# Kernel optimization log

Measured on AMD Instinct MI355X. Metric: run time of the kernel, lower is better.

Reference implementation:

```python
import jax, jax.numpy as jnp
import numpy as np

NB_HEAD = 16
SIZE_PER_HEAD = 64
D_MODEL = 1024
B, SQ, SK = 4, 2048, 2048


def setup_inputs() -> dict:
    key = jax.random.key(0)
    ks = jax.random.split(key, 8)
    Q_seq = jax.random.normal(ks[0], (B, SQ, D_MODEL), dtype=jnp.float32)
    K_seq = jax.random.normal(ks[1], (B, SK, D_MODEL), dtype=jnp.float32)
    V_seq = jax.random.normal(ks[2], (B, SK, D_MODEL), dtype=jnp.float32)
    Q_len = jax.random.randint(ks[3], (B, 1), 0, SQ, dtype=jnp.int32)
    V_len = jax.random.randint(ks[4], (B, 1), 0, SK, dtype=jnp.int32)
    out_dim = NB_HEAD * SIZE_PER_HEAD
    scale = float(np.sqrt(6.0 / (D_MODEL + out_dim)))  # glorot_uniform
    WQ = jax.random.uniform(ks[5], (D_MODEL, out_dim), jnp.float32, -scale, scale)
    WK = jax.random.uniform(ks[6], (D_MODEL, out_dim), jnp.float32, -scale, scale)
    WV = jax.random.uniform(ks[7], (D_MODEL, out_dim), jnp.float32, -scale, scale)
    return {"Q_seq": Q_seq, "K_seq": K_seq, "V_seq": V_seq,
            "Q_len": Q_len, "V_len": V_len, "WQ": WQ, "WK": WK, "WV": WV}


def reference(Q_seq, K_seq, V_seq, Q_len, V_len, WQ, WK, WV):
    b, sq, _ = Q_seq.shape
    sk = K_seq.shape[1]
    H, D = NB_HEAD, SIZE_PER_HEAD
    # projections -> [B, H, S, D]
    Q = (Q_seq @ WQ).reshape(b, sq, H, D).transpose(0, 2, 1, 3)
    K = (K_seq @ WK).reshape(b, sk, H, D).transpose(0, 2, 1, 3)
    V = (V_seq @ WV).reshape(b, sk, H, D).transpose(0, 2, 1, 3)
    # scaled dot-product scores [B, H, Sq, Sk]
    A = jnp.einsum('bhqd,bhkd->bhqk', Q, K) / jnp.float32(np.sqrt(D))
    # faithful to original Mask (no cumsum): masks ONLY the key position == V_len
    vmask = jax.nn.one_hot(V_len[:, 0], sk, dtype=A.dtype)  # [B, Sk]
    A = A - vmask[:, None, None, :] * jnp.float32(1e12)
    A = jax.nn.softmax(A, axis=-1)
    out = jnp.einsum('bhqk,bhkd->bhqd', A, V)
    out = out.transpose(0, 2, 1, 3).reshape(b, sq, H * D)
    # multiplicative mask: zeros ONLY the query position == Q_len
    qmask = 1.0 - jax.nn.one_hot(Q_len[:, 0], sq, dtype=out.dtype)  # [B, Sq]
    return out * qmask[:, :, None]
```

## Files before the change

kernel.cpp:

```cpp
#include <hip/hip_runtime.h>
#include <hip/hip_bf16.h>

typedef float f32x4 __attribute__((ext_vector_type(4)));
typedef float f32x16 __attribute__((ext_vector_type(16)));
typedef short bf16x8 __attribute__((ext_vector_type(8)));
typedef unsigned short u16;
typedef u16 u16x4 __attribute__((ext_vector_type(4)));
typedef u16 u16x8 __attribute__((ext_vector_type(8)));
typedef unsigned u32;
typedef unsigned u32x2 __attribute__((ext_vector_type(2)));

#define GLDS(gp, lp) __builtin_amdgcn_global_load_lds( \
    (const __attribute__((address_space(1))) void*)(gp), \
    (__attribute__((address_space(3))) void*)(lp), 16, 0, 0)

__device__ __forceinline__ u16 f2bf(float f) {
  union { float f; unsigned u; } v; v.f = f;
  unsigned r = v.u + 0x7fffu + ((v.u >> 16) & 1u);
  return (u16)(r >> 16);
}

__device__ __forceinline__ u32 cvtpk(float lo, float hi) {
  u32 r;
  asm("v_cvt_pk_bf16_f32 %0, %1, %2" : "=v"(r) : "v"(lo), "v"(hi));
  return r;
}

__device__ __forceinline__ float exp2i(float x) {
  float r;
  asm("v_exp_f32 %0, %1" : "=v"(r) : "v"(x));
  return r;
}

__global__ __launch_bounds__(256) void ktrans(const float* __restrict__ WQ,
                                              const float* __restrict__ WK,
                                              const float* __restrict__ WV,
                                              u16* __restrict__ Wt) {
  int z = blockIdx.z;
  const float* W = (z == 0) ? WQ : (z == 1) ? WK : WV;
  u16* o = Wt + (size_t)z * 1024 * 1024;
  float scale = (z == 0) ? 0.18033688f : 1.0f;
  __shared__ float tl[32][33];
  int tx = threadIdx.x & 31, ty = threadIdx.x >> 5;
  int ko = blockIdx.x * 32, no = blockIdx.y * 32;
#pragma unroll
  for (int i = 0; i < 32; i += 8)
    tl[ty + i][tx] = W[(size_t)(ko + ty + i) * 1024 + no + tx];
  __syncthreads();
#pragma unroll
  for (int i = 0; i < 32; i += 8)
    o[(size_t)(no + ty + i) * 1024 + ko + tx] = f2bf(tl[tx][ty + i] * scale);
}

__global__ __launch_bounds__(256) void kconv(const float* __restrict__ A, u16* __restrict__ Ab) {
  int tid = blockIdx.x * 256 + threadIdx.x;
  size_t base = (size_t)tid * 16;
  const f32x4* p = (const f32x4*)(A + base);
  f32x4 v0 = p[0], v1 = p[1], v2 = p[2], v3 = p[3];
  union { u32 u[8]; u16x8 h[2]; } pk;
  pk.u[0] = cvtpk(v0.x, v0.y); pk.u[1] = cvtpk(v0.z, v0.w);
  pk.u[2] = cvtpk(v1.x, v1.y); pk.u[3] = cvtpk(v1.z, v1.w);
  pk.u[4] = cvtpk(v2.x, v2.y); pk.u[5] = cvtpk(v2.z, v2.w);
  pk.u[6] = cvtpk(v3.x, v3.y); pk.u[7] = cvtpk(v3.z, v3.w);
  *(u16x8*)(Ab + base) = pk.h[0];
  *(u16x8*)(Ab + base + 8) = pk.h[1];
}

__global__ __launch_bounds__(256, 3) void kproj(
    const u16* __restrict__ Ab, const u16* __restrict__ Wz,
    u16* __restrict__ O, int isV) {
  __shared__ __align__(16) u16 lds[16384];
  int t = threadIdx.x, lane = t & 63, w = t >> 6;
  int wm = (w >> 1) * 64, wn = (w & 1) * 64;
  int f = blockIdx.y * 8 + blockIdx.x;
  int x_t = (f >> 3) & 7;
  int y_t = (f & 7) | ((f >> 6) << 3);
  int m0 = y_t * 128, n0 = x_t * 128;
  f32x4 acc[4][4];
#pragma unroll
  for (int i = 0; i < 4; ++i)
#pragma unroll
    for (int j = 0; j < 4; ++j) acc[i][j] = (f32x4){0.f, 0.f, 0.f, 0.f};

  int srow = t >> 3, sk8 = (t & 7) << 3;
  int lbw = w * 512;
  const u16* gA = Ab + (size_t)(m0 + srow) * 1024 + (sk8 ^ ((srow & 7) << 3));
  const u16* gB = Wz + (size_t)(n0 + srow) * 1024 + (sk8 ^ ((srow & 7) << 3));

  for (int k0 = 0; k0 < 1024; k0 += 64) {
    __syncthreads();
#pragma unroll
    for (int p = 0; p < 4; ++p) GLDS(gA + p * 32768 + k0, &lds[p * 2048 + lbw]);
#pragma unroll
    for (int p = 0; p < 4; ++p) GLDS(gB + p * 32768 + k0, &lds[8192 + p * 2048 + lbw]);
    __syncthreads();
#pragma unroll
    for (int kk = 0; kk < 64; kk += 32) {
      int ko8 = kk + ((lane >> 4) << 3);
      bf16x8 af[4], bfr[4];
#pragma unroll
      for (int mi = 0; mi < 4; ++mi) {
        int r = wm + mi * 16 + (lane & 15);
        af[mi] = *(const bf16x8*)(&lds[r * 64 + (ko8 ^ ((r & 7) << 3))]);
      }
#pragma unroll
      for (int ni = 0; ni < 4; ++ni) {
        int r = wn + ni * 16 + (lane & 15);
        bfr[ni] = *(const bf16x8*)(&lds[8192 + r * 64 + (ko8 ^ ((r & 7) << 3))]);
      }
#pragma unroll
      for (int mi = 0; mi < 4; ++mi)
#pragma unroll
        for (int ni = 0; ni < 4; ++ni)
          acc[mi][ni] = __builtin_amdgcn_mfma_f32_16x16x32_bf16(af[mi], bfr[ni], acc[mi][ni], 0, 0, 0);
    }
  }
  int bb = m0 >> 11;
  if (!isV) {
#pragma unroll
    for (int mi = 0; mi < 4; ++mi) {
      int m4 = m0 + wm + mi * 16 + ((lane >> 4) << 2);
      int s4 = m4 & 2047;
#pragma unroll
      for (int ni = 0; ni < 4; ++ni) {
        int n = n0 + wn + ni * 16 + (lane & 15);
        int hh = n >> 6, d = n & 63;
        u16* op = O + (((size_t)(bb * 16 + hh) * 2048 + s4) * 64 + d);
#pragma unroll
        for (int j = 0; j < 4; ++j) op[(size_t)j * 64] = f2bf(acc[mi][ni][j]);
      }
    }
  } else {
#pragma unroll
    for (int mi = 0; mi < 4; ++mi) {
      int m4 = m0 + wm + mi * 16 + ((lane >> 4) << 2);
      int s4 = m4 & 2047;
#pragma unroll
      for (int ni = 0; ni < 4; ++ni) {
        int n = n0 + wn + ni * 16 + (lane & 15);
        int hh = n >> 6, d = n & 63;
        u16x4 pv = {f2bf(acc[mi][ni][0]), f2bf(acc[mi][ni][1]),
                    f2bf(acc[mi][ni][2]), f2bf(acc[mi][ni][3])};
        *(u16x4*)(&O[((size_t)(bb * 16 + hh) * 64 + d) * 2048 + s4]) = pv;
      }
    }
  }
}

__global__ __launch_bounds__(512, 4) void kattn(
    const u16* __restrict__ Qw, const u16* __restrict__ Kw, const u16* __restrict__ Vt,
    const int* __restrict__ Qlen, const int* __restrict__ Vlen, float* __restrict__ out) {
  int fid = blockIdx.x;
  int bh = (fid & 7) * 8 + (fid >> 6);
  int qx = (fid >> 3) & 7;
  int b = bh >> 4, h = bh & 15;
  int q0 = qx * 256;
  int t = threadIdx.x, lane = t & 63, w = t >> 6, hi = lane >> 5, ln = lane & 31;
  __shared__ __align__(16) u16 smem[16384];
  const int qlen = Qlen[b], vlen = Vlen[b];

  const u16* Qp = Qw + ((size_t)bh * 2048 + q0 + w * 32 + ln) * 64;
  bf16x8 qf[4];
#pragma unroll
  for (int r = 0; r < 4; ++r) qf[r] = *(const bf16x8*)(Qp + r * 16 + hi * 8);

  int srow = t >> 3;
  int sks = (((t & 7) << 4) ^ ((srow & 7) << 4)) >> 1;
  const u16* gK = Kw + ((size_t)bh * 2048 + srow) * 64 + sks;
  const u16* gV = Vt + ((size_t)bh * 64 + srow) * 2048 + sks;
  int lbw = (t >> 6) * 512;

  GLDS(gK, &smem[lbw]);
  GLDS(gV, &smem[4096 + lbw]);

  float Lloc = 0.f;
  f32x16 o0, o1;
#pragma unroll
  for (int i = 0; i < 16; ++i) { o0[i] = 0.f; o1[i] = 0.f; }
  __syncthreads();

  for (int kt = 0; kt < 32; ++kt) {
    int qb = (kt & 1) * 8192;
    int nb = ((kt & 1) ^ 1) * 8192;
    if (kt < 31) {
      GLDS(gK + (size_t)(kt + 1) * 4096, &smem[nb + lbw]);
      GLDS(gV + (kt + 1) * 64, &smem[nb + 4096 + lbw]);
    }
    f32x16 sa[2];
#pragma unroll
    for (int kb = 0; kb < 2; ++kb)
#pragma unroll
      for (int i = 0; i < 16; ++i) sa[kb][i] = 0.f;
    __builtin_amdgcn_s_setprio(1);
#pragma unroll
    for (int kb = 0; kb < 2; ++kb) {
      int row = kb * 32 + ln;
      int rs7 = (row & 7) << 4;
#pragma unroll
      for (int r = 0; r < 4; ++r) {
        int byt = row * 128 + ((r * 32 + hi * 16) ^ rs7);
        bf16x8 kf = *(const bf16x8*)(&smem[qb + (byt >> 1)]);
        sa[kb] = __builtin_amdgcn_mfma_f32_32x32x16_bf16(kf, qf[r], sa[kb], 0, 0, 0);
      }
    }
    __builtin_amdgcn_s_setprio(0);
    if ((vlen >> 6) == kt) {
#pragma unroll
      for (int kb = 0; kb < 2; ++kb)
#pragma unroll
        for (int i = 0; i < 16; ++i) {
          int kv = (kt << 6) + kb * 32 + ((i & 3) + ((i >> 2) << 3)) + (hi << 2);
          if (kv == vlen) sa[kb][i] = -1e12f;
        }
    }
    float r0 = 0.f, r1 = 0.f, r2 = 0.f, r3 = 0.f;
#pragma unroll
    for (int kb = 0; kb < 2; ++kb)
#pragma unroll
      for (int i = 0; i < 16; i += 4) {
        float p0 = exp2i(sa[kb][i]);     sa[kb][i] = p0;     r0 += p0;
        float p1 = exp2i(sa[kb][i + 1]); sa[kb][i + 1] = p1; r1 += p1;
        float p2 = exp2i(sa[kb][i + 2]); sa[kb][i + 2] = p2; r2 += p2;
        float p3 = exp2i(sa[kb][i + 3]); sa[kb][i + 3] = p3; r3 += p3;
      }
    Lloc += (r0 + r1) + (r2 + r3);
    bf16x8 pf[4];
#pragma unroll
    for (int kb = 0; kb < 2; ++kb)
#pragma unroll
      for (int ff = 0; ff < 2; ++ff) {
        u32 a0 = cvtpk(sa[kb][8 * ff + 0], sa[kb][8 * ff + 1]);
        u32 b0 = cvtpk(sa[kb][8 * ff + 4], sa[kb][8 * ff + 5]);
        u32x2 q0v = __builtin_amdgcn_permlane32_swap(a0, b0, false, false);
        u32 a1 = cvtpk(sa[kb][8 * ff + 2], sa[kb][8 * ff + 3]);
        u32 b1 = cvtpk(sa[kb][8 * ff + 6], sa[kb][8 * ff + 7]);
        u32x2 q1v = __builtin_amdgcn_permlane32_swap(a1, b1, false, false);
        union { u32 u[4]; bf16x8 v; } uu;
        uu.u[0] = q0v.x; uu.u[1] = q1v.x; uu.u[2] = q0v.y; uu.u[3] = q1v.y;
        pf[kb * 2 + ff] = uu.v;
      }
    __builtin_amdgcn_s_setprio(1);
#pragma unroll
    for (int db = 0; db < 2; ++db) {
      int row = db * 32 + ln;
      int rs7 = (row & 7) << 4;
#pragma unroll
      for (int s4 = 0; s4 < 4; ++s4) {
        int byt = row * 128 + ((s4 * 32 + hi * 16) ^ rs7);
        bf16x8 vf = *(const bf16x8*)(&smem[qb + 4096 + (byt >> 1)]);
        if (db == 0) o0 = __builtin_amdgcn_mfma_f32_32x32x16_bf16(vf, pf[s4], o0, 0, 0, 0);
        else         o1 = __builtin_amdgcn_mfma_f32_32x32x16_bf16(vf, pf[s4], o1, 0, 0, 0);
      }
    }
    __builtin_amdgcn_s_setprio(0);
    __syncthreads();
  }
  float Lt = Lloc + __shfl_xor(Lloc, 32, 64);
  int q = q0 + w * 32 + ln;
  float inv = (q == qlen) ? 0.f : 1.f / Lt;
  float* op = out + ((size_t)b * 2048 + q) * 1024 + h * 64;
#pragma unroll
  for (int g = 0; g < 4; ++g) {
    f32x4 v0 = {o0[4 * g + 0] * inv, o0[4 * g + 1] * inv, o0[4 * g + 2] * inv, o0[4 * g + 3] * inv};
    *(f32x4*)(op + g * 8 + hi * 4) = v0;
    f32x4 v1 = {o1[4 * g + 0] * inv, o1[4 * g + 1] * inv, o1[4 * g + 2] * inv, o1[4 * g + 3] * inv};
    *(f32x4*)(op + 32 + g * 8 + hi * 4) = v1;
  }
}

extern "C" void kernel_launch(void* const* d_in, const int* in_sizes, int n_in,
                              void* d_out, int out_size, void* d_ws, size_t ws_size,
                              hipStream_t stream) {
  (void)in_sizes; (void)n_in; (void)out_size; (void)ws_size;
  const float* Qs = (const float*)d_in[0];
  const float* Ks = (const float*)d_in[1];
  const float* Vs = (const float*)d_in[2];
  const int* Ql = (const int*)d_in[3];
  const int* Vl = (const int*)d_in[4];
  const float* WQ = (const float*)d_in[5];
  const float* WK = (const float*)d_in[6];
  const float* WV = (const float*)d_in[7];
  float* out = (float*)d_out;

  const size_t M1 = 1024 * 1024;
  u16* Wt = (u16*)d_ws;
  u16* Qw = Wt + 3 * M1;
  u16* Kw = Qw + 8 * M1;
  u16* Vtw = Kw + 8 * M1;
  u16* Ab = Vtw + 8 * M1;

  ktrans<<<dim3(32, 32, 3), 256, 0, stream>>>(WQ, WK, WV, Wt);
  kconv<<<2048, 256, 0, stream>>>(Qs, Ab);
  kproj<<<dim3(8, 64), 256, 0, stream>>>(Ab, Wt, Qw, 0);
  kconv<<<2048, 256, 0, stream>>>(Ks, Ab);
  kproj<<<dim3(8, 64), 256, 0, stream>>>(Ab, Wt + M1, Kw, 0);
  kconv<<<2048, 256, 0, stream>>>(Vs, Ab);
  kproj<<<dim3(8, 64), 256, 0, stream>>>(Ab, Wt + 2 * M1, Vtw, 1);
  kattn<<<512, 512, 0, stream>>>(Qw, Kw, Vtw, Ql, Vl, out);
}
```

Measured before the change: 303.3 us.

## Batch Q/K/V conversion and projection launches; deepen attention K/V prefetch to two tiles

The three conversion kernels and three projection GEMMs are merged into single launches indexed by a grid dimension. The bf16 copies of Q and K inputs are staged in the output buffer so all three can live at once. In the attention kernel, each pipeline stage now loads two 64-key K/V tiles, doubling LDS to 64KB and halving the number of block barriers. Fewer launches and fuller grids should cut launch gaps and tail effects, but the larger LDS footprint may reduce attention occupancy.

```diff
diff --git a/kernel.cpp b/kernel.cpp
--- a/kernel.cpp
+++ b/kernel.cpp
@@ -52,7 +52,15 @@
     o[(size_t)(no + ty + i) * 1024 + ko + tx] = f2bf(tl[tx][ty + i] * scale);
 }
 
-__global__ __launch_bounds__(256) void kconv(const float* __restrict__ A, u16* __restrict__ Ab) {
+__global__ __launch_bounds__(256) void kconv3(const float* __restrict__ A0,
+                                              const float* __restrict__ A1,
+                                              const float* __restrict__ A2,
+                                              u16* __restrict__ B0,
+                                              u16* __restrict__ B1,
+                                              u16* __restrict__ B2) {
+  int z = blockIdx.y;
+  const float* A = (z == 0) ? A0 : (z == 1) ? A1 : A2;
+  u16* Ab = (z == 0) ? B0 : (z == 1) ? B1 : B2;
   int tid = blockIdx.x * 256 + threadIdx.x;
   size_t base = (size_t)tid * 16;
   const f32x4* p = (const f32x4*)(A + base);
@@ -67,8 +75,13 @@
 }
 
 __global__ __launch_bounds__(256, 3) void kproj(
-    const u16* __restrict__ Ab, const u16* __restrict__ Wz,
-    u16* __restrict__ O, int isV) {
+    const u16* __restrict__ Ab0, const u16* __restrict__ Ab1, const u16* __restrict__ Ab2,
+    const u16* __restrict__ Wt, u16* __restrict__ Qw, u16* __restrict__ Kw,
+    u16* __restrict__ Vtw) {
+  int z = blockIdx.z;
+  const u16* Ab = (z == 0) ? Ab0 : (z == 1) ? Ab1 : Ab2;
+  const u16* Wz = Wt + (size_t)z * 1024 * 1024;
+  u16* O = (z == 0) ? Qw : (z == 1) ? Kw : Vtw;
   __shared__ __align__(16) u16 lds[16384];
   int t = threadIdx.x, lane = t & 63, w = t >> 6;
   int wm = (w >> 1) * 64, wn = (w & 1) * 64;
@@ -116,7 +129,7 @@
     }
   }
   int bb = m0 >> 11;
-  if (!isV) {
+  if (z < 2) {
 #pragma unroll
     for (int mi = 0; mi < 4; ++mi) {
       int m4 = m0 + wm + mi * 16 + ((lane >> 4) << 2);
@@ -156,7 +169,7 @@
   int b = bh >> 4, h = bh & 15;
   int q0 = qx * 256;
   int t = threadIdx.x, lane = t & 63, w = t >> 6, hi = lane >> 5, ln = lane & 31;
-  __shared__ __align__(16) u16 smem[16384];
+  __shared__ __align__(16) u16 smem[32768];
   const int qlen = Qlen[b], vlen = Vlen[b];
 
   const u16* Qp = Qw + ((size_t)bh * 2048 + q0 + w * 32 + ln) * 64;
@@ -172,6 +185,8 @@
 
   GLDS(gK, &smem[lbw]);
   GLDS(gV, &smem[4096 + lbw]);
+  GLDS(gK + 4096, &smem[8192 + lbw]);
+  GLDS(gV + 64, &smem[12288 + lbw]);
 
   float Lloc = 0.f;
   f32x16 o0, o1;
@@ -179,80 +194,87 @@
   for (int i = 0; i < 16; ++i) { o0[i] = 0.f; o1[i] = 0.f; }
   __syncthreads();
 
-  for (int kt = 0; kt < 32; ++kt) {
-    int qb = (kt & 1) * 8192;
-    int nb = ((kt & 1) ^ 1) * 8192;
-    if (kt < 31) {
-      GLDS(gK + (size_t)(kt + 1) * 4096, &smem[nb + lbw]);
-      GLDS(gV + (kt + 1) * 64, &smem[nb + 4096 + lbw]);
-    }
-    f32x16 sa[2];
-#pragma unroll
-    for (int kb = 0; kb < 2; ++kb)
-#pragma unroll
-      for (int i = 0; i < 16; ++i) sa[kb][i] = 0.f;
-    __builtin_amdgcn_s_setprio(1);
-#pragma unroll
-    for (int kb = 0; kb < 2; ++kb) {
-      int row = kb * 32 + ln;
-      int rs7 = (row & 7) << 4;
-#pragma unroll
-      for (int r = 0; r < 4; ++r) {
-        int byt = row * 128 + ((r * 32 + hi * 16) ^ rs7);
-        bf16x8 kf = *(const bf16x8*)(&smem[qb + (byt >> 1)]);
-        sa[kb] = __builtin_amdgcn_mfma_f32_32x32x16_bf16(kf, qf[r], sa[kb], 0, 0, 0);
-      }
-    }
-    __builtin_amdgcn_s_setprio(0);
-    if ((vlen >> 6) == kt) {
+  for (int kt = 0; kt < 16; ++kt) {
+    int qb = (kt & 1) << 14;
+    int nb = qb ^ 16384;
+    if (kt < 15) {
+      GLDS(gK + (size_t)(2 * kt + 2) * 4096, &smem[nb + lbw]);
+      GLDS(gV + (2 * kt + 2) * 64, &smem[nb + 4096 + lbw]);
+      GLDS(gK + (size_t)(2 * kt + 3) * 4096, &smem[nb + 8192 + lbw]);
+      GLDS(gV + (2 * kt + 3) * 64, &smem[nb + 12288 + lbw]);
+    }
+#pragma unroll
+    for (int u = 0; u < 2; ++u) {
+      int tb = qb + u * 8192;
+      int tau = 2 * kt + u;
+      f32x16 sa[2];
 #pragma unroll
       for (int kb = 0; kb < 2; ++kb)
 #pragma unroll
-        for (int i = 0; i < 16; ++i) {
-          int kv = (kt << 6) + kb * 32 + ((i & 3) + ((i >> 2) << 3)) + (hi << 2);
-          if (kv == vlen) sa[kb][i] = -1e12f;
+        for (int i = 0; i < 16; ++i) sa[kb][i] = 0.f;
+      __builtin_amdgcn_s_setprio(1);
+#pragma unroll
+      for (int kb = 0; kb < 2; ++kb) {
+        int row = kb * 32 + ln;
+        int rs7 = (row & 7) << 4;
+#pragma unroll
+        for (int r = 0; r < 4; ++r) {
+          int byt = row * 128 + ((r * 32 + hi * 16) ^ rs7);
+          bf16x8 kf = *(const bf16x8*)(&smem[tb + (byt >> 1)]);
+          sa[kb] = __builtin_amdgcn_mfma_f32_32x32x16_bf16(kf, qf[r], sa[kb], 0, 0, 0);
         }
-    }
-    float r0 = 0.f, r1 = 0.f, r2 = 0.f, r3 = 0.f;
-#pragma unroll
-    for (int kb = 0; kb < 2; ++kb)
-#pragma unroll
-      for (int i = 0; i < 16; i += 4) {
-        float p0 = exp2i(sa[kb][i]);     sa[kb][i] = p0;     r0 += p0;
-        float p1 = exp2i(sa[kb][i + 1]); sa[kb][i + 1] = p1; r1 += p1;
-        float p2 = exp2i(sa[kb][i + 2]); sa[kb][i + 2] = p2; r2 += p2;
-        float p3 = exp2i(sa[kb][i + 3]); sa[kb][i + 3] = p3; r3 += p3;
-      }
-    Lloc += (r0 + r1) + (r2 + r3);
-    bf16x8 pf[4];
-#pragma unroll
-    for (int kb = 0; kb < 2; ++kb)
-#pragma unroll
-      for (int ff = 0; ff < 2; ++ff) {
-        u32 a0 = cvtpk(sa[kb][8 * ff + 0], sa[kb][8 * ff + 1]);
-        u32 b0 = cvtpk(sa[kb][8 * ff + 4], sa[kb][8 * ff + 5]);
-        u32x2 q0v = __builtin_amdgcn_permlane32_swap(a0, b0, false, false);
-        u32 a1 = cvtpk(sa[kb][8 * ff + 2], sa[kb][8 * ff + 3]);
-        u32 b1 = cvtpk(sa[kb][8 * ff + 6], sa[kb][8 * ff + 7]);
-        u32x2 q1v = __builtin_amdgcn_permlane32_swap(a1, b1, false, false);
-        union { u32 u[4]; bf16x8 v; } uu;
-        uu.u[0] = q0v.x; uu.u[1] = q1v.x; uu.u[2] = q0v.y; uu.u[3] = q1v.y;
-        pf[kb * 2 + ff] = uu.v;
-      }
-    __builtin_amdgcn_s_setprio(1);
-#pragma unroll
-    for (int db = 0; db < 2; ++db) {
-      int row = db * 32 + ln;
-      int rs7 = (row & 7) << 4;
-#pragma unroll
-      for (int s4 = 0; s4 < 4; ++s4) {
-        int byt = row * 128 + ((s4 * 32 + hi * 16) ^ rs7);
-        bf16x8 vf = *(const bf16x8*)(&smem[qb + 4096 + (byt >> 1)]);
-        if (db == 0) o0 = __builtin_amdgcn_mfma_f32_32x32x16_bf16(vf, pf[s4], o0, 0, 0, 0);
-        else         o1 = __builtin_amdgcn_mfma_f32_32x32x16_bf16(vf, pf[s4], o1, 0, 0, 0);
-      }
-    }
-    __builtin_amdgcn_s_setprio(0);
+      }
+      __builtin_amdgcn_s_setprio(0);
+      if ((vlen >> 6) == tau) {
+#pragma unroll
+        for (int kb = 0; kb < 2; ++kb)
+#pragma unroll
+          for (int i = 0; i < 16; ++i) {
+            int kv = (tau << 6) + kb * 32 + ((i & 3) + ((i >> 2) << 3)) + (hi << 2);
+            if (kv == vlen) sa[kb][i] = -1e12f;
+          }
+      }
+      float r0 = 0.f, r1 = 0.f, r2 = 0.f, r3 = 0.f;
+#pragma unroll
+      for (int kb = 0; kb < 2; ++kb)
+#pragma unroll
+        for (int i = 0; i < 16; i += 4) {
+          float p0 = exp2i(sa[kb][i]);     sa[kb][i] = p0;     r0 += p0;
+          float p1 = exp2i(sa[kb][i + 1]); sa[kb][i + 1] = p1; r1 += p1;
+          float p2 = exp2i(sa[kb][i + 2]); sa[kb][i + 2] = p2; r2 += p2;
+          float p3 = exp2i(sa[kb][i + 3]); sa[kb][i + 3] = p3; r3 += p3;
+        }
+      Lloc += (r0 + r1) + (r2 + r3);
+      bf16x8 pf[4];
+#pragma unroll
+      for (int kb = 0; kb < 2; ++kb)
+#pragma unroll
+        for (int ff = 0; ff < 2; ++ff) {
+          u32 a0 = cvtpk(sa[kb][8 * ff + 0], sa[kb][8 * ff + 1]);
+          u32 b0 = cvtpk(sa[kb][8 * ff + 4], sa[kb][8 * ff + 5]);
+          u32x2 q0v = __builtin_amdgcn_permlane32_swap(a0, b0, false, false);
+          u32 a1 = cvtpk(sa[kb][8 * ff + 2], sa[kb][8 * ff + 3]);
+          u32 b1 = cvtpk(sa[kb][8 * ff + 6], sa[kb][8 * ff + 7]);
+          u32x2 q1v = __builtin_amdgcn_permlane32_swap(a1, b1, false, false);
+          union { u32 u[4]; bf16x8 v; } uu;
+          uu.u[0] = q0v.x; uu.u[1] = q1v.x; uu.u[2] = q0v.y; uu.u[3] = q1v.y;
+          pf[kb * 2 + ff] = uu.v;
+        }
+      __builtin_amdgcn_s_setprio(1);
+#pragma unroll
+      for (int db = 0; db < 2; ++db) {
+        int row = db * 32 + ln;
+        int rs7 = (row & 7) << 4;
+#pragma unroll
+        for (int s4 = 0; s4 < 4; ++s4) {
+          int byt = row * 128 + ((s4 * 32 + hi * 16) ^ rs7);
+          bf16x8 vf = *(const bf16x8*)(&smem[tb + 4096 + (byt >> 1)]);
+          if (db == 0) o0 = __builtin_amdgcn_mfma_f32_32x32x16_bf16(vf, pf[s4], o0, 0, 0, 0);
+          else         o1 = __builtin_amdgcn_mfma_f32_32x32x16_bf16(vf, pf[s4], o1, 0, 0, 0);
+        }
+      }
+      __builtin_amdgcn_s_setprio(0);
+    }
     __syncthreads();
   }
   float Lt = Lloc + __shfl_xor(Lloc, 32, 64);
@@ -287,14 +309,12 @@
   u16* Qw = Wt + 3 * M1;
   u16* Kw = Qw + 8 * M1;
   u16* Vtw = Kw + 8 * M1;
-  u16* Ab = Vtw + 8 * M1;
+  u16* Ab2 = Vtw + 8 * M1;
+  u16* Ab0 = (u16*)d_out;
+  u16* Ab1 = Ab0 + 8 * M1;
 
   ktrans<<<dim3(32, 32, 3), 256, 0, stream>>>(WQ, WK, WV, Wt);
-  kconv<<<2048, 256, 0, stream>>>(Qs, Ab);
-  kproj<<<dim3(8, 64), 256, 0, stream>>>(Ab, Wt, Qw, 0);
-  kconv<<<2048, 256, 0, stream>>>(Ks, Ab);
-  kproj<<<dim3(8, 64), 256, 0, stream>>>(Ab, Wt + M1, Kw, 0);
-  kconv<<<2048, 256, 0, stream>>>(Vs, Ab);
-  kproj<<<dim3(8, 64), 256, 0, stream>>>(Ab, Wt + 2 * M1, Vtw, 1);
+  kconv3<<<dim3(2048, 3), 256, 0, stream>>>(Qs, Ks, Vs, Ab0, Ab1, Ab2);
+  kproj<<<dim3(8, 64, 3), 256, 0, stream>>>(Ab0, Ab1, Ab2, Wt, Qw, Kw, Vtw);
   kattn<<<512, 512, 0, stream>>>(Qw, Kw, Vtw, Ql, Vl, out);
 }
```

New measurement: 312.9 us. 1.03x slower.

## Fuse fp32-to-bf16 activation conversion into projection GEMM and batch three projections

Applied to the files above, without the earlier changes.

Removes the separate conversion kernels that wrote bf16 copies of Q/K/V inputs, instead loading fp32 tiles into LDS via global_load_lds and converting to bf16 when building MFMA fragments. The three projection GEMMs are launched as one grid using blockIdx.z. This avoids writing and re-reading intermediate bf16 buffers and two launches, at the cost of larger LDS usage, doubled A-tile global bytes, and redundant per-block conversions.

```diff
diff --git a/kernel.cpp b/kernel.cpp
--- a/kernel.cpp
+++ b/kernel.cpp
@@ -52,24 +52,16 @@
     o[(size_t)(no + ty + i) * 1024 + ko + tx] = f2bf(tl[tx][ty + i] * scale);
 }
 
-__global__ __launch_bounds__(256) void kconv(const float* __restrict__ A, u16* __restrict__ Ab) {
-  int tid = blockIdx.x * 256 + threadIdx.x;
-  size_t base = (size_t)tid * 16;
-  const f32x4* p = (const f32x4*)(A + base);
-  f32x4 v0 = p[0], v1 = p[1], v2 = p[2], v3 = p[3];
-  union { u32 u[8]; u16x8 h[2]; } pk;
-  pk.u[0] = cvtpk(v0.x, v0.y); pk.u[1] = cvtpk(v0.z, v0.w);
-  pk.u[2] = cvtpk(v1.x, v1.y); pk.u[3] = cvtpk(v1.z, v1.w);
-  pk.u[4] = cvtpk(v2.x, v2.y); pk.u[5] = cvtpk(v2.z, v2.w);
-  pk.u[6] = cvtpk(v3.x, v3.y); pk.u[7] = cvtpk(v3.z, v3.w);
-  *(u16x8*)(Ab + base) = pk.h[0];
-  *(u16x8*)(Ab + base + 8) = pk.h[1];
-}
-
 __global__ __launch_bounds__(256, 3) void kproj(
-    const u16* __restrict__ Ab, const u16* __restrict__ Wz,
-    u16* __restrict__ O, int isV) {
-  __shared__ __align__(16) u16 lds[16384];
+    const float* __restrict__ A0, const float* __restrict__ A1, const float* __restrict__ A2,
+    const u16* __restrict__ Wt, u16* __restrict__ Qw, u16* __restrict__ Kw,
+    u16* __restrict__ Vtw) {
+  int z = blockIdx.z;
+  const float* A = (z == 0) ? A0 : (z == 1) ? A1 : A2;
+  const u16* Wz = Wt + (size_t)z * 1024 * 1024;
+  u16* O = (z == 0) ? Qw : (z == 1) ? Kw : Vtw;
+  __shared__ __align__(16) float ldsA[8192];
+  __shared__ __align__(16) u16 ldsB[8192];
   int t = threadIdx.x, lane = t & 63, w = t >> 6;
   int wm = (w >> 1) * 64, wn = (w & 1) * 64;
   int f = blockIdx.y * 8 + blockIdx.x;
@@ -82,17 +74,19 @@
 #pragma unroll
     for (int j = 0; j < 4; ++j) acc[i][j] = (f32x4){0.f, 0.f, 0.f, 0.f};
 
+  int srow16 = t >> 4, sk4 = (t & 15) << 2;
   int srow = t >> 3, sk8 = (t & 7) << 3;
-  int lbw = w * 512;
-  const u16* gA = Ab + (size_t)(m0 + srow) * 1024 + (sk8 ^ ((srow & 7) << 3));
+  const float* gA = A + (size_t)(m0 + srow16) * 1024 + (sk4 ^ ((srow16 & 7) << 2));
   const u16* gB = Wz + (size_t)(n0 + srow) * 1024 + (sk8 ^ ((srow & 7) << 3));
+  int lbwA = w * 256;
+  int lbwB = w * 512;
 
   for (int k0 = 0; k0 < 1024; k0 += 64) {
     __syncthreads();
 #pragma unroll
-    for (int p = 0; p < 4; ++p) GLDS(gA + p * 32768 + k0, &lds[p * 2048 + lbw]);
-#pragma unroll
-    for (int p = 0; p < 4; ++p) GLDS(gB + p * 32768 + k0, &lds[8192 + p * 2048 + lbw]);
+    for (int p = 0; p < 8; ++p) GLDS(gA + p * 16384 + k0, &ldsA[p * 1024 + lbwA]);
+#pragma unroll
+    for (int p = 0; p < 4; ++p) GLDS(gB + p * 32768 + k0, &ldsB[p * 2048 + lbwB]);
     __syncthreads();
 #pragma unroll
     for (int kk = 0; kk < 64; kk += 32) {
@@ -101,12 +95,18 @@
 #pragma unroll
       for (int mi = 0; mi < 4; ++mi) {
         int r = wm + mi * 16 + (lane & 15);
-        af[mi] = *(const bf16x8*)(&lds[r * 64 + (ko8 ^ ((r & 7) << 3))]);
+        int sw = (r & 7) << 2;
+        f32x4 alo = *(const f32x4*)(&ldsA[r * 64 + (ko8 ^ sw)]);
+        f32x4 ahi = *(const f32x4*)(&ldsA[r * 64 + ((ko8 + 4) ^ sw)]);
+        union { u32 u[4]; bf16x8 v; } pk;
+        pk.u[0] = cvtpk(alo.x, alo.y); pk.u[1] = cvtpk(alo.z, alo.w);
+        pk.u[2] = cvtpk(ahi.x, ahi.y); pk.u[3] = cvtpk(ahi.z, ahi.w);
+        af[mi] = pk.v;
       }
 #pragma unroll
       for (int ni = 0; ni < 4; ++ni) {
         int r = wn + ni * 16 + (lane & 15);
-        bfr[ni] = *(const bf16x8*)(&lds[8192 + r * 64 + (ko8 ^ ((r & 7) << 3))]);
+        bfr[ni] = *(const bf16x8*)(&ldsB[r * 64 + (ko8 ^ ((r & 7) << 3))]);
       }
 #pragma unroll
       for (int mi = 0; mi < 4; ++mi)
@@ -116,7 +116,7 @@
     }
   }
   int bb = m0 >> 11;
-  if (!isV) {
+  if (z < 2) {
 #pragma unroll
     for (int mi = 0; mi < 4; ++mi) {
       int m4 = m0 + wm + mi * 16 + ((lane >> 4) << 2);
@@ -287,14 +287,8 @@
   u16* Qw = Wt + 3 * M1;
   u16* Kw = Qw + 8 * M1;
   u16* Vtw = Kw + 8 * M1;
-  u16* Ab = Vtw + 8 * M1;
 
   ktrans<<<dim3(32, 32, 3), 256, 0, stream>>>(WQ, WK, WV, Wt);
-  kconv<<<2048, 256, 0, stream>>>(Qs, Ab);
-  kproj<<<dim3(8, 64), 256, 0, stream>>>(Ab, Wt, Qw, 0);
-  kconv<<<2048, 256, 0, stream>>>(Ks, Ab);
-  kproj<<<dim3(8, 64), 256, 0, stream>>>(Ab, Wt + M1, Kw, 0);
-  kconv<<<2048, 256, 0, stream>>>(Vs, Ab);
-  kproj<<<dim3(8, 64), 256, 0, stream>>>(Ab, Wt + 2 * M1, Vtw, 1);
+  kproj<<<dim3(8, 64, 3), 256, 0, stream>>>(Qs, Ks, Vs, Wt, Qw, Kw, Vtw);
   kattn<<<512, 512, 0, stream>>>(Qw, Kw, Vtw, Ql, Vl, out);
 }
```

Measured after the change: 293.4 us. 3.3% less time.
